# Performance work log

Measured on AMD Instinct MI355X. Metric: run time of the kernel, lower is better.

## Reference

```python
import jax, jax.numpy as jnp
import numpy as np

HEAD_DIM = 128
NEG_INF = -1e10


def setup_inputs() -> dict:
    key = jax.random.key(0)
    k1, k2, k3, k4 = jax.random.split(key, 4)
    B, T, C, D = 4, 4096, 1024, HEAD_DIM
    x = jax.random.normal(k1, (B, T, C), dtype=jnp.float32)
    # nn.Linear(C, D, bias=False) weight is [D, C]; we store transposed [C, D]
    Wq = jax.random.normal(k2, (C, D), dtype=jnp.float32) * (1.0 / np.sqrt(C))
    Wk = jax.random.normal(k3, (C, D), dtype=jnp.float32) * (1.0 / np.sqrt(C))
    Wv = jax.random.normal(k4, (C, D), dtype=jnp.float32) * (1.0 / np.sqrt(C))
    return {"x": x, "Wq": Wq, "Wk": Wk, "Wv": Wv}


def reference(x, Wq, Wk, Wv):
    B, T, C = x.shape
    D = Wq.shape[1]
    Q = jnp.einsum("btc,cd->btd", x, Wq)
    K = jnp.einsum("btc,cd->btd", x, Wk)
    V = jnp.einsum("btc,cd->btd", x, Wv)
    scores = jnp.einsum("bqd,bkd->bqk", Q, K) * (1.0 / np.sqrt(D))
    causal = jnp.tril(jnp.ones((T, T), dtype=bool))  # [T, T]
    scores = jnp.where(causal, scores, NEG_INF)
    probs = jax.nn.softmax(scores, axis=-1)
    out = jnp.einsum("bqk,bkd->bqd", probs, V)
    return out
```

## Files before the change

kernel.cpp:

```cpp
#include <hip/hip_runtime.h>
#include <hip/hip_bf16.h>
#include <stdint.h>
#include <math.h>


typedef __attribute__((ext_vector_type(4))) float f32x4;
typedef __attribute__((ext_vector_type(8))) short bf16x8;
typedef __attribute__((ext_vector_type(4))) unsigned short u16x4;

#define NBATCH 4
#define NT 4096
#define NC 1024
#define ND 128
#define BT (NBATCH * NT)
#define NSPLIT 8
#define KSPAN (NT / NSPLIT)

#define EXP2F(x) __builtin_amdgcn_exp2f(x)

__device__ __forceinline__ unsigned short f2bf(float f) {
  union { float f; uint32_t u; } v; v.f = f;
  uint32_t u = v.u;
  return (unsigned short)((u + 0x7FFFu + ((u >> 16) & 1u)) >> 16);
}

__device__ __forceinline__ float bf2f(unsigned short h) {
  union { uint32_t u; float f; } v; v.u = ((uint32_t)h) << 16;
  return v.f;
}

__device__ __forceinline__ bf16x8 cvt8(const f32x4 a0, const f32x4 a1) {
  bf16x8 r;
  r[0] = (short)f2bf(a0[0]); r[1] = (short)f2bf(a0[1]);
  r[2] = (short)f2bf(a0[2]); r[3] = (short)f2bf(a0[3]);
  r[4] = (short)f2bf(a1[0]); r[5] = (short)f2bf(a1[1]);
  r[6] = (short)f2bf(a1[2]); r[7] = (short)f2bf(a1[3]);
  return r;
}

__device__ __forceinline__ void g2lds16(const void* g, void* l) {
  __builtin_amdgcn_global_load_lds(
      (const __attribute__((address_space(1))) unsigned int*)g,
      (__attribute__((address_space(3))) unsigned int*)l, 16, 0, 0);
}

__global__ void wcvt_kernel(const float* __restrict__ Wq, const float* __restrict__ Wk,
                            const float* __restrict__ Wv, unsigned short* __restrict__ Wt) {
  const float CK = 0.12751744f;
  int idx = blockIdx.x * blockDim.x + threadIdx.x;
  int m = idx >> 17;
  int r = idx & 131071;
  int d = r >> 10;
  int c = r & 1023;
  const float* W = (m == 0) ? Wq : (m == 1) ? Wk : Wv;
  float v = W[c * ND + d];
  if (m == 1) v *= CK;
  Wt[idx] = f2bf(v);
}

__global__ __launch_bounds__(256, 3)
void proj_kernel(const float* __restrict__ x, const unsigned short* __restrict__ Wt,
                 unsigned short* __restrict__ Qb, unsigned short* __restrict__ Kb,
                 unsigned short* __restrict__ Vt) {
  __shared__ char smem[2][16384];

  int w = threadIdx.x >> 6;
  int lane = threadIdx.x & 63;
  int r16 = lane & 15;
  int h4 = lane >> 4;
  int wm = w & 1;
  int wn = w >> 1;

  int mt = blockIdx.x & 255;
  int nt = blockIdx.x >> 8;

  const char* xg = (const char*)(x + (size_t)(mt * 64) * NC);
  const char* wg = (const char*)(Wt + (size_t)(nt * 128) * NC);

  f32x4 acc[2][4];
  #pragma unroll
  for (int m = 0; m < 2; ++m)
    #pragma unroll
    for (int n = 0; n < 4; ++n) acc[m][n] = (f32x4){0.f, 0.f, 0.f, 0.f};

  int cA0 = (w * 2 + 0) * 64 + lane;
  int cA1 = (w * 2 + 1) * 64 + lane;

  #define STAGE(buf, t)                                                          \
    {                                                                            \
      int c0 = (t) * 32;                                                         \
      {                                                                          \
        int c = cA0, row = c >> 3, s = c & 7;                                    \
        g2lds16(xg + (size_t)row * 4096 + c0 * 4 + ((s ^ (row & 7)) << 4),       \
                smem[buf] + (w * 2 + 0) * 1024);                                 \
      }                                                                          \
      {                                                                          \
        int c = cA1, row = c >> 3, s = c & 7;                                    \
        g2lds16(xg + (size_t)row * 4096 + c0 * 4 + ((s ^ (row & 7)) << 4),       \
                smem[buf] + (w * 2 + 1) * 1024);                                 \
      }                                                                          \
      {                                                                          \
        int c = cA0, row = c >> 2, s = c & 3;                                    \
        g2lds16(wg + (size_t)row * 2048 + c0 * 2 + ((s ^ (row & 3)) << 4),       \
                smem[buf] + 8192 + (w * 2 + 0) * 1024);                          \
      }                                                                          \
      {                                                                          \
        int c = cA1, row = c >> 2, s = c & 3;                                    \
        g2lds16(wg + (size_t)row * 2048 + c0 * 2 + ((s ^ (row & 3)) << 4),       \
                smem[buf] + 8192 + (w * 2 + 1) * 1024);                          \
      }                                                                          \
    }

  STAGE(0, 0);
  __syncthreads();

  for (int t = 0; t < 32; ++t) {
    int cur = t & 1;
    if (t + 1 < 32) STAGE(cur ^ 1, t + 1);

    bf16x8 af[2];
    #pragma unroll
    for (int m = 0; m < 2; ++m) {
      int row = wm * 32 + m * 16 + r16;
      f32x4 a0 = *(const f32x4*)(smem[cur] + row * 128 + (((h4 * 2) ^ (row & 7)) << 4));
      f32x4 a1 = *(const f32x4*)(smem[cur] + row * 128 + (((h4 * 2 + 1) ^ (row & 7)) << 4));
      af[m] = cvt8(a0, a1);
    }
    __builtin_amdgcn_s_setprio(1);
    #pragma unroll
    for (int n = 0; n < 4; ++n) {
      int brow = wn * 64 + n * 16 + r16;
      bf16x8 bfr = *(const bf16x8*)(smem[cur] + 8192 + brow * 64 + ((h4 ^ (brow & 3)) << 4));
      acc[0][n] = __builtin_amdgcn_mfma_f32_16x16x32_bf16(af[0], bfr, acc[0][n], 0, 0, 0);
      acc[1][n] = __builtin_amdgcn_mfma_f32_16x16x32_bf16(af[1], bfr, acc[1][n], 0, 0, 0);
    }
    __builtin_amdgcn_s_setprio(0);
    __syncthreads();
  }
  #undef STAGE

  if (nt < 2) {
    unsigned short* dst = (nt == 0) ? Qb : Kb;
    #pragma unroll
    for (int m = 0; m < 2; ++m) {
      int t0 = mt * 64 + wm * 32 + m * 16 + h4 * 4;
      #pragma unroll
      for (int n = 0; n < 4; ++n) {
        int d = wn * 64 + n * 16 + r16;
        #pragma unroll
        for (int r = 0; r < 4; ++r)
          dst[(size_t)(t0 + r) * ND + d] = f2bf(acc[m][n][r]);
      }
    }
  } else {
    #pragma unroll
    for (int m = 0; m < 2; ++m) {
      int t0 = mt * 64 + wm * 32 + m * 16 + h4 * 4;
      int b = t0 >> 12;
      int tl = t0 & (NT - 1);
      #pragma unroll
      for (int n = 0; n < 4; ++n) {
        int d = wn * 64 + n * 16 + r16;
        u16x4 pk;
        #pragma unroll
        for (int r = 0; r < 4; ++r) pk[r] = f2bf(acc[m][n][r]);
        *(u16x4*)(Vt + (size_t)b * (ND * NT) + (size_t)d * NT + tl) = pk;
      }
    }
  }
}

__global__ __launch_bounds__(256, 2)
void attn_kernel(const unsigned short* __restrict__ Qb,
                 const unsigned short* __restrict__ Kb,
                 const unsigned short* __restrict__ Vt,
                 unsigned short* __restrict__ Opart, float* __restrict__ Mpart,
                 float* __restrict__ Lpart) {
  __shared__ unsigned short kbuf[64 * 128];
  __shared__ unsigned short vbuf[128 * 64];
  __shared__ unsigned short plds[4][32][72];

  int wave = threadIdx.x >> 6;
  int lane = threadIdx.x & 63;
  int r16 = lane & 15;
  int h4 = lane >> 4;
  int h8 = h4 * 8;

  int l = blockIdx.x;
  int b = l & 3;
  int u = l >> 2;
  int a = (int)((sqrtf(2.0f * (float)u + 1.0f) - 1.0f) * 0.5f);
  if (a < 0) a = 0;
  while (2 * (a + 1) * (a + 2) <= u) ++a;
  while (a > 0 && 2 * a * (a + 1) > u) --a;
  int rem = u - 2 * a * (a + 1);
  int apl = a + 1;
  int rr = rem / apl;
  int s = rem - rr * apl;
  int qbt = 4 * a + rr;

  int qb0 = qbt * 128;
  int z = s;
  int kstart = s << 9;
  int kend = min(qb0 + 128, kstart + KSPAN);

  int q0 = qb0 + wave * 32;

  const unsigned short* Qbb = Qb + (size_t)b * NT * ND;
  const unsigned short* Kbb = Kb + (size_t)b * NT * ND;
  const unsigned short* Vtb = Vt + (size_t)b * ND * NT;

  bf16x8 qf[2][4];
  #pragma unroll
  for (int f = 0; f < 2; ++f)
    #pragma unroll
    for (int dc = 0; dc < 4; ++dc)
      qf[f][dc] = *(const bf16x8*)(Qbb + (size_t)(q0 + f * 16 + r16) * ND + dc * 32 + h8);

  f32x4 accO[2][8];
  #pragma unroll
  for (int f = 0; f < 2; ++f)
    #pragma unroll
    for (int i = 0; i < 8; ++i) accO[f][i] = (f32x4){0.f, 0.f, 0.f, 0.f};
  float mr[2][4], lr[2][4];
  #pragma unroll
  for (int f = 0; f < 2; ++f)
    #pragma unroll
    for (int r = 0; r < 4; ++r) { mr[f][r] = -1e30f; lr[f][r] = 0.f; }

  for (int kv0 = kstart; kv0 < kend; kv0 += 64) {
    #pragma unroll
    for (int i = 0; i < 4; ++i) {
      int e = i * 256 + wave * 64 + lane;
      int krow = e >> 4, ks = e & 15;
      const char* gk = (const char*)(Kbb + (size_t)(kv0 + krow) * ND)
                       + ((ks * 16) ^ ((krow & 7) << 4));
      g2lds16(gk, (char*)kbuf + (size_t)(i * 256 + wave * 64) * 16);
    }
    #pragma unroll
    for (int i = 0; i < 4; ++i) {
      int e = i * 256 + wave * 64 + lane;
      int vrow = e >> 3, vs = e & 7;
      const char* gv = (const char*)(Vtb + (size_t)vrow * NT + kv0)
                       + ((vs * 16) ^ ((vrow & 7) << 4));
      g2lds16(gv, (char*)vbuf + (size_t)(i * 256 + wave * 64) * 16);
    }
    __syncthreads();

    if (kv0 < q0 + 32) {
      f32x4 s2[2][4];
      __builtin_amdgcn_s_setprio(1);
      #pragma unroll
      for (int kt = 0; kt < 4; ++kt) {
        s2[0][kt] = (f32x4){0.f, 0.f, 0.f, 0.f};
        s2[1][kt] = (f32x4){0.f, 0.f, 0.f, 0.f};
        int krow = kt * 16 + r16;
        #pragma unroll
        for (int dc = 0; dc < 4; ++dc) {
          int off = krow * 256 + ((dc * 64 + h4 * 16) ^ ((krow & 7) << 4));
          bf16x8 kf = *(const bf16x8*)((const char*)kbuf + off);
          s2[0][kt] = __builtin_amdgcn_mfma_f32_16x16x32_bf16(qf[0][dc], kf, s2[0][kt], 0, 0, 0);
          s2[1][kt] = __builtin_amdgcn_mfma_f32_16x16x32_bf16(qf[1][dc], kf, s2[1][kt], 0, 0, 0);
        }
      }
      __builtin_amdgcn_s_setprio(0);

      float pmax[2][4];
      #pragma unroll
      for (int f = 0; f < 2; ++f)
        #pragma unroll
        for (int r = 0; r < 4; ++r) pmax[f][r] = -3e38f;
      if (kv0 + 63 <= q0) {
        #pragma unroll
        for (int kt = 0; kt < 4; ++kt)
          #pragma unroll
          for (int f = 0; f < 2; ++f)
            #pragma unroll
            for (int r = 0; r < 4; ++r) pmax[f][r] = fmaxf(pmax[f][r], s2[f][kt][r]);
      } else {
        #pragma unroll
        for (int kt = 0; kt < 4; ++kt) {
          int key = kv0 + kt * 16 + r16;
          #pragma unroll
          for (int f = 0; f < 2; ++f)
            #pragma unroll
            for (int r = 0; r < 4; ++r) {
              int q = q0 + f * 16 + h4 * 4 + r;
              float v = (key <= q) ? s2[f][kt][r] : -3e38f;
              s2[f][kt][r] = v;
              pmax[f][r] = fmaxf(pmax[f][r], v);
            }
        }
      }

      bool grow = false;
      #pragma unroll
      for (int f = 0; f < 2; ++f)
        #pragma unroll
        for (int r = 0; r < 4; ++r) grow = grow || (pmax[f][r] > mr[f][r] + 11.0f);
      if (__any(grow)) {
        #pragma unroll
        for (int f = 0; f < 2; ++f) {
          float sf[4];
          #pragma unroll
          for (int r = 0; r < 4; ++r) {
            #pragma unroll
            for (int msk = 1; msk < 16; msk <<= 1)
              pmax[f][r] = fmaxf(pmax[f][r], __shfl_xor(pmax[f][r], msk, 64));
            float mn = fmaxf(mr[f][r], pmax[f][r]);
            sf[r] = EXP2F(mr[f][r] - mn);
            mr[f][r] = mn;
            lr[f][r] *= sf[r];
          }
          #pragma unroll
          for (int dt = 0; dt < 8; ++dt) {
            #pragma unroll
            for (int r = 0; r < 4; ++r) accO[f][dt][r] *= sf[r];
          }
        }
      }

      #pragma unroll
      for (int kt = 0; kt < 4; ++kt)
        #pragma unroll
        for (int f = 0; f < 2; ++f)
          #pragma unroll
          for (int r = 0; r < 4; ++r) {
            float p = EXP2F(s2[f][kt][r] - mr[f][r]);
            s2[f][kt][r] = p;
            lr[f][r] += p;
          }

      #pragma unroll
      for (int kt = 0; kt < 4; ++kt)
        #pragma unroll
        for (int f = 0; f < 2; ++f)
          #pragma unroll
          for (int r = 0; r < 4; ++r)
            plds[wave][f * 16 + h4 * 4 + r][kt * 16 + r16] = f2bf(s2[f][kt][r]);

      __builtin_amdgcn_s_setprio(1);
      #pragma unroll
      for (int kc = 0; kc < 2; ++kc) {
        bf16x8 pf0 = *(const bf16x8*)(&plds[wave][r16][kc * 32 + h8]);
        bf16x8 pf1 = *(const bf16x8*)(&plds[wave][16 + r16][kc * 32 + h8]);
        #pragma unroll
        for (int dt = 0; dt < 8; ++dt) {
          int vrow = dt * 16 + r16;
          int off = vrow * 128 + ((kc * 64 + h4 * 16) ^ ((vrow & 7) << 4));
          bf16x8 vf = *(const bf16x8*)((const char*)vbuf + off);
          accO[0][dt] = __builtin_amdgcn_mfma_f32_16x16x32_bf16(pf0, vf, accO[0][dt], 0, 0, 0);
          accO[1][dt] = __builtin_amdgcn_mfma_f32_16x16x32_bf16(pf1, vf, accO[1][dt], 0, 0, 0);
        }
      }
      __builtin_amdgcn_s_setprio(0);
    }
    __syncthreads();
  }

  #pragma unroll
  for (int f = 0; f < 2; ++f)
    #pragma unroll
    for (int r = 0; r < 4; ++r)
      #pragma unroll
      for (int msk = 1; msk < 16; msk <<= 1)
        lr[f][r] += __shfl_xor(lr[f][r], msk, 64);

  size_t pbase = ((size_t)z * NBATCH + b) * NT + q0;
  #pragma unroll
  for (int f = 0; f < 2; ++f)
    #pragma unroll
    for (int dt = 0; dt < 8; ++dt)
      #pragma unroll
      for (int r = 0; r < 4; ++r)
        Opart[(pbase + f * 16 + h4 * 4 + r) * ND + dt * 16 + r16] = f2bf(accO[f][dt][r]);
  if (r16 == 0) {
    #pragma unroll
    for (int f = 0; f < 2; ++f)
      #pragma unroll
      for (int r = 0; r < 4; ++r) {
        Mpart[pbase + f * 16 + h4 * 4 + r] = mr[f][r];
        Lpart[pbase + f * 16 + h4 * 4 + r] = lr[f][r];
      }
  }
}

__global__ void merge_kernel(const unsigned short* __restrict__ Opart,
                             const float* __restrict__ Mpart,
                             const float* __restrict__ Lpart, float* __restrict__ out) {
  int idx = blockIdx.x * blockDim.x + threadIdx.x;
  int bq = idx >> 4;
  int dg = idx & 15;
  int q = bq & (NT - 1);
  int nz = (q >> 9) + 1;

  float M = -3e38f;
  #pragma unroll
  for (int zz = 0; zz < NSPLIT; ++zz)
    if (zz < nz) M = fmaxf(M, Mpart[(size_t)zz * BT + bq]);

  float denom = 0.f;
  float o[8] = {0.f, 0.f, 0.f, 0.f, 0.f, 0.f, 0.f, 0.f};
  #pragma unroll
  for (int zz = 0; zz < NSPLIT; ++zz) {
    if (zz < nz) {
      float e = EXP2F(Mpart[(size_t)zz * BT + bq] - M);
      denom += e * Lpart[(size_t)zz * BT + bq];
      bf16x8 ov = *(const bf16x8*)(Opart + ((size_t)zz * BT + bq) * ND + dg * 8);
      #pragma unroll
      for (int j = 0; j < 8; ++j) o[j] += e * bf2f((unsigned short)ov[j]);
    }
  }
  float inv = 1.0f / denom;
  f32x4 o0, o1;
  #pragma unroll
  for (int j = 0; j < 4; ++j) { o0[j] = o[j] * inv; o1[j] = o[4 + j] * inv; }
  float* dst = out + (size_t)bq * ND + dg * 8;
  *(f32x4*)dst = o0;
  *(f32x4*)(dst + 4) = o1;
}

extern "C" void kernel_launch(void* const* d_in, const int* in_sizes, int n_in,
                              void* d_out, int out_size, void* d_ws, size_t ws_size,
                              hipStream_t stream) {
  const float* x  = (const float*)d_in[0];
  const float* Wq = (const float*)d_in[1];
  const float* Wk = (const float*)d_in[2];
  const float* Wv = (const float*)d_in[3];

  char* ws = (char*)d_ws;
  unsigned short* Qb = (unsigned short*)ws;
  unsigned short* Kb = (unsigned short*)(ws + 4194304);
  unsigned short* Vt = (unsigned short*)(ws + 8388608);
  unsigned short* Opart = (unsigned short*)(ws + 12582912);
  float* Mpart = (float*)(ws + 46137344);
  float* Lpart = (float*)(ws + 46661632);
  unsigned short* Wt = (unsigned short*)(ws + 12582912);

  hipLaunchKernelGGL(wcvt_kernel, dim3(1536), dim3(256), 0, stream, Wq, Wk, Wv, Wt);
  hipLaunchKernelGGL(proj_kernel, dim3(768), dim3(256), 0, stream, x, Wt, Qb, Kb, Vt);
  hipLaunchKernelGGL(attn_kernel, dim3(576), dim3(256), 0, stream,
                     Qb, Kb, Vt, Opart, Mpart, Lpart);
  hipLaunchKernelGGL(merge_kernel, dim3(BT * 16 / 256), dim3(256), 0, stream,
                     Opart, Mpart, Lpart, (float*)d_out);
}
```

Before: 86.38 us.

## Map waves to batches and read K/V fragments directly from global memory

```diff
diff --git a/kernel.cpp b/kernel.cpp
--- a/kernel.cpp
+++ b/kernel.cpp
@@ -176,8 +176,6 @@
                  const unsigned short* __restrict__ Vt,
                  unsigned short* __restrict__ Opart, float* __restrict__ Mpart,
                  float* __restrict__ Lpart) {
-  __shared__ unsigned short kbuf[64 * 128];
-  __shared__ unsigned short vbuf[128 * 64];
   __shared__ unsigned short plds[4][32][72];
 
   int wave = threadIdx.x >> 6;
@@ -186,25 +184,20 @@
   int h4 = lane >> 4;
   int h8 = h4 * 8;
 
-  int l = blockIdx.x;
-  int b = l & 3;
-  int u = l >> 2;
-  int a = (int)((sqrtf(2.0f * (float)u + 1.0f) - 1.0f) * 0.5f);
-  if (a < 0) a = 0;
-  while (2 * (a + 1) * (a + 2) <= u) ++a;
-  while (a > 0 && 2 * a * (a + 1) > u) --a;
-  int rem = u - 2 * a * (a + 1);
-  int apl = a + 1;
-  int rr = rem / apl;
-  int s = rem - rr * apl;
-  int qbt = 4 * a + rr;
-
-  int qb0 = qbt * 128;
+  int b = wave;
+  int u = blockIdx.x;
+  int g = (int)((sqrtf(4.0f + 2.0f * (float)u) - 2.0f) * 0.25f);
+  if (g < 0) g = 0;
+  while (8 * (g + 1) * (g + 2) <= u) ++g;
+  while (g > 0 && 8 * g * (g + 1) > u) --g;
+  int rem = u - 8 * g * (g + 1);
+  int qt = 16 * g + rem / (g + 1);
+  int s = rem % (g + 1);
+
+  int q0 = qt * 32;
   int z = s;
   int kstart = s << 9;
-  int kend = min(qb0 + 128, kstart + KSPAN);
-
-  int q0 = qb0 + wave * 32;
+  int kend = min(q0 + 32, kstart + KSPAN);
 
   const unsigned short* Qbb = Qb + (size_t)b * NT * ND;
   const unsigned short* Kbb = Kb + (size_t)b * NT * ND;
@@ -229,133 +222,109 @@
     for (int r = 0; r < 4; ++r) { mr[f][r] = -1e30f; lr[f][r] = 0.f; }
 
   for (int kv0 = kstart; kv0 < kend; kv0 += 64) {
-    #pragma unroll
-    for (int i = 0; i < 4; ++i) {
-      int e = i * 256 + wave * 64 + lane;
-      int krow = e >> 4, ks = e & 15;
-      const char* gk = (const char*)(Kbb + (size_t)(kv0 + krow) * ND)
-                       + ((ks * 16) ^ ((krow & 7) << 4));
-      g2lds16(gk, (char*)kbuf + (size_t)(i * 256 + wave * 64) * 16);
-    }
-    #pragma unroll
-    for (int i = 0; i < 4; ++i) {
-      int e = i * 256 + wave * 64 + lane;
-      int vrow = e >> 3, vs = e & 7;
-      const char* gv = (const char*)(Vtb + (size_t)vrow * NT + kv0)
-                       + ((vs * 16) ^ ((vrow & 7) << 4));
-      g2lds16(gv, (char*)vbuf + (size_t)(i * 256 + wave * 64) * 16);
-    }
-    __syncthreads();
-
-    if (kv0 < q0 + 32) {
-      f32x4 s2[2][4];
-      __builtin_amdgcn_s_setprio(1);
+    f32x4 s2[2][4];
+    __builtin_amdgcn_s_setprio(1);
+    #pragma unroll
+    for (int kt = 0; kt < 4; ++kt) {
+      s2[0][kt] = (f32x4){0.f, 0.f, 0.f, 0.f};
+      s2[1][kt] = (f32x4){0.f, 0.f, 0.f, 0.f};
+      const unsigned short* krow = Kbb + (size_t)(kv0 + kt * 16 + r16) * ND;
+      #pragma unroll
+      for (int dc = 0; dc < 4; ++dc) {
+        bf16x8 kf = *(const bf16x8*)(krow + dc * 32 + h8);
+        s2[0][kt] = __builtin_amdgcn_mfma_f32_16x16x32_bf16(qf[0][dc], kf, s2[0][kt], 0, 0, 0);
+        s2[1][kt] = __builtin_amdgcn_mfma_f32_16x16x32_bf16(qf[1][dc], kf, s2[1][kt], 0, 0, 0);
+      }
+    }
+    __builtin_amdgcn_s_setprio(0);
+
+    float pmax[2][4];
+    #pragma unroll
+    for (int f = 0; f < 2; ++f)
+      #pragma unroll
+      for (int r = 0; r < 4; ++r) pmax[f][r] = -3e38f;
+    if (kv0 + 63 <= q0) {
+      #pragma unroll
+      for (int kt = 0; kt < 4; ++kt)
+        #pragma unroll
+        for (int f = 0; f < 2; ++f)
+          #pragma unroll
+          for (int r = 0; r < 4; ++r) pmax[f][r] = fmaxf(pmax[f][r], s2[f][kt][r]);
+    } else {
       #pragma unroll
       for (int kt = 0; kt < 4; ++kt) {
-        s2[0][kt] = (f32x4){0.f, 0.f, 0.f, 0.f};
-        s2[1][kt] = (f32x4){0.f, 0.f, 0.f, 0.f};
-        int krow = kt * 16 + r16;
-        #pragma unroll
-        for (int dc = 0; dc < 4; ++dc) {
-          int off = krow * 256 + ((dc * 64 + h4 * 16) ^ ((krow & 7) << 4));
-          bf16x8 kf = *(const bf16x8*)((const char*)kbuf + off);
-          s2[0][kt] = __builtin_amdgcn_mfma_f32_16x16x32_bf16(qf[0][dc], kf, s2[0][kt], 0, 0, 0);
-          s2[1][kt] = __builtin_amdgcn_mfma_f32_16x16x32_bf16(qf[1][dc], kf, s2[1][kt], 0, 0, 0);
-        }
-      }
-      __builtin_amdgcn_s_setprio(0);
-
-      float pmax[2][4];
-      #pragma unroll
-      for (int f = 0; f < 2; ++f)
-        #pragma unroll
-        for (int r = 0; r < 4; ++r) pmax[f][r] = -3e38f;
-      if (kv0 + 63 <= q0) {
-        #pragma unroll
-        for (int kt = 0; kt < 4; ++kt)
-          #pragma unroll
-          for (int f = 0; f < 2; ++f)
-            #pragma unroll
-            for (int r = 0; r < 4; ++r) pmax[f][r] = fmaxf(pmax[f][r], s2[f][kt][r]);
-      } else {
-        #pragma unroll
-        for (int kt = 0; kt < 4; ++kt) {
-          int key = kv0 + kt * 16 + r16;
-          #pragma unroll
-          for (int f = 0; f < 2; ++f)
-            #pragma unroll
-            for (int r = 0; r < 4; ++r) {
-              int q = q0 + f * 16 + h4 * 4 + r;
-              float v = (key <= q) ? s2[f][kt][r] : -3e38f;
-              s2[f][kt][r] = v;
-              pmax[f][r] = fmaxf(pmax[f][r], v);
-            }
-        }
-      }
-
-      bool grow = false;
-      #pragma unroll
-      for (int f = 0; f < 2; ++f)
-        #pragma unroll
-        for (int r = 0; r < 4; ++r) grow = grow || (pmax[f][r] > mr[f][r] + 11.0f);
-      if (__any(grow)) {
-        #pragma unroll
-        for (int f = 0; f < 2; ++f) {
-          float sf[4];
-          #pragma unroll
-          for (int r = 0; r < 4; ++r) {
-            #pragma unroll
-            for (int msk = 1; msk < 16; msk <<= 1)
-              pmax[f][r] = fmaxf(pmax[f][r], __shfl_xor(pmax[f][r], msk, 64));
-            float mn = fmaxf(mr[f][r], pmax[f][r]);
-            sf[r] = EXP2F(mr[f][r] - mn);
-            mr[f][r] = mn;
-            lr[f][r] *= sf[r];
-          }
-          #pragma unroll
-          for (int dt = 0; dt < 8; ++dt) {
-            #pragma unroll
-            for (int r = 0; r < 4; ++r) accO[f][dt][r] *= sf[r];
-          }
-        }
-      }
-
-      #pragma unroll
-      for (int kt = 0; kt < 4; ++kt)
+        int key = kv0 + kt * 16 + r16;
         #pragma unroll
         for (int f = 0; f < 2; ++f)
           #pragma unroll
           for (int r = 0; r < 4; ++r) {
-            float p = EXP2F(s2[f][kt][r] - mr[f][r]);
-            s2[f][kt][r] = p;
-            lr[f][r] += p;
+            int q = q0 + f * 16 + h4 * 4 + r;
+            float v = (key <= q) ? s2[f][kt][r] : -3e38f;
+            s2[f][kt][r] = v;
+            pmax[f][r] = fmaxf(pmax[f][r], v);
           }
-
-      #pragma unroll
-      for (int kt = 0; kt < 4; ++kt)
-        #pragma unroll
-        for (int f = 0; f < 2; ++f)
+      }
+    }
+
+    bool grow = false;
+    #pragma unroll
+    for (int f = 0; f < 2; ++f)
+      #pragma unroll
+      for (int r = 0; r < 4; ++r) grow = grow || (pmax[f][r] > mr[f][r] + 11.0f);
+    if (__any(grow)) {
+      #pragma unroll
+      for (int f = 0; f < 2; ++f) {
+        float sf[4];
+        #pragma unroll
+        for (int r = 0; r < 4; ++r) {
           #pragma unroll
-          for (int r = 0; r < 4; ++r)
-            plds[wave][f * 16 + h4 * 4 + r][kt * 16 + r16] = f2bf(s2[f][kt][r]);
-
-      __builtin_amdgcn_s_setprio(1);
-      #pragma unroll
-      for (int kc = 0; kc < 2; ++kc) {
-        bf16x8 pf0 = *(const bf16x8*)(&plds[wave][r16][kc * 32 + h8]);
-        bf16x8 pf1 = *(const bf16x8*)(&plds[wave][16 + r16][kc * 32 + h8]);
+          for (int msk = 1; msk < 16; msk <<= 1)
+            pmax[f][r] = fmaxf(pmax[f][r], __shfl_xor(pmax[f][r], msk, 64));
+          float mn = fmaxf(mr[f][r], pmax[f][r]);
+          sf[r] = EXP2F(mr[f][r] - mn);
+          mr[f][r] = mn;
+          lr[f][r] *= sf[r];
+        }
         #pragma unroll
         for (int dt = 0; dt < 8; ++dt) {
-          int vrow = dt * 16 + r16;
-          int off = vrow * 128 + ((kc * 64 + h4 * 16) ^ ((vrow & 7) << 4));
-          bf16x8 vf = *(const bf16x8*)((const char*)vbuf + off);
-          accO[0][dt] = __builtin_amdgcn_mfma_f32_16x16x32_bf16(pf0, vf, accO[0][dt], 0, 0, 0);
-          accO[1][dt] = __builtin_amdgcn_mfma_f32_16x16x32_bf16(pf1, vf, accO[1][dt], 0, 0, 0);
+          #pragma unroll
+          for (int r = 0; r < 4; ++r) accO[f][dt][r] *= sf[r];
         }
       }
-      __builtin_amdgcn_s_setprio(0);
-    }
-    __syncthreads();
+    }
+
+    #pragma unroll
+    for (int kt = 0; kt < 4; ++kt)
+      #pragma unroll
+      for (int f = 0; f < 2; ++f)
+        #pragma unroll
+        for (int r = 0; r < 4; ++r) {
+          float p = EXP2F(s2[f][kt][r] - mr[f][r]);
+          s2[f][kt][r] = p;
+          lr[f][r] += p;
+        }
+
+    #pragma unroll
+    for (int kt = 0; kt < 4; ++kt)
+      #pragma unroll
+      for (int f = 0; f < 2; ++f)
+        #pragma unroll
+        for (int r = 0; r < 4; ++r)
+          plds[wave][f * 16 + h4 * 4 + r][kt * 16 + r16] = f2bf(s2[f][kt][r]);
+
+    __builtin_amdgcn_s_setprio(1);
+    #pragma unroll
+    for (int kc = 0; kc < 2; ++kc) {
+      bf16x8 pf0 = *(const bf16x8*)(&plds[wave][r16][kc * 32 + h8]);
+      bf16x8 pf1 = *(const bf16x8*)(&plds[wave][16 + r16][kc * 32 + h8]);
+      #pragma unroll
+      for (int dt = 0; dt < 8; ++dt) {
+        bf16x8 vf = *(const bf16x8*)(Vtb + (size_t)(dt * 16 + r16) * NT + kv0 + kc * 32 + h8);
+        accO[0][dt] = __builtin_amdgcn_mfma_f32_16x16x32_bf16(pf0, vf, accO[0][dt], 0, 0, 0);
+        accO[1][dt] = __builtin_amdgcn_mfma_f32_16x16x32_bf16(pf1, vf, accO[1][dt], 0, 0, 0);
+      }
+    }
+    __builtin_amdgcn_s_setprio(0);
   }
 
   #pragma unroll
```

Measured after the change: 154.1 us. +78.4%, slower.

## Compute transposed score tiles so softmax row stats live per lane

Applied to the files above, without the earlier changes.

```diff
diff --git a/kernel.cpp b/kernel.cpp
--- a/kernel.cpp
+++ b/kernel.cpp
@@ -7,6 +7,7 @@
 typedef __attribute__((ext_vector_type(4))) float f32x4;
 typedef __attribute__((ext_vector_type(8))) short bf16x8;
 typedef __attribute__((ext_vector_type(4))) unsigned short u16x4;
+typedef __attribute__((ext_vector_type(2))) unsigned int u32x2;
 
 #define NBATCH 4
 #define NT 4096
@@ -35,6 +36,12 @@
   r[2] = (short)f2bf(a0[2]); r[3] = (short)f2bf(a0[3]);
   r[4] = (short)f2bf(a1[0]); r[5] = (short)f2bf(a1[1]);
   r[6] = (short)f2bf(a1[2]); r[7] = (short)f2bf(a1[3]);
+  return r;
+}
+
+__device__ __forceinline__ unsigned int cvtpk(float a, float b) {
+  unsigned int r;
+  asm("v_cvt_pk_bf16_f32 %0, %1, %2" : "=v"(r) : "v"(a), "v"(b));
   return r;
 }
 
@@ -222,11 +229,8 @@
   for (int f = 0; f < 2; ++f)
     #pragma unroll
     for (int i = 0; i < 8; ++i) accO[f][i] = (f32x4){0.f, 0.f, 0.f, 0.f};
-  float mr[2][4], lr[2][4];
-  #pragma unroll
-  for (int f = 0; f < 2; ++f)
-    #pragma unroll
-    for (int r = 0; r < 4; ++r) { mr[f][r] = -1e30f; lr[f][r] = 0.f; }
+  float mr[2] = {-1e30f, -1e30f};
+  float lr[2] = {0.f, 0.f};
 
   for (int kv0 = kstart; kv0 < kend; kv0 += 64) {
     #pragma unroll
@@ -248,96 +252,88 @@
     __syncthreads();
 
     if (kv0 < q0 + 32) {
-      f32x4 s2[2][4];
+      f32x4 sT[2][4];
       __builtin_amdgcn_s_setprio(1);
       #pragma unroll
       for (int kt = 0; kt < 4; ++kt) {
-        s2[0][kt] = (f32x4){0.f, 0.f, 0.f, 0.f};
-        s2[1][kt] = (f32x4){0.f, 0.f, 0.f, 0.f};
+        sT[0][kt] = (f32x4){0.f, 0.f, 0.f, 0.f};
+        sT[1][kt] = (f32x4){0.f, 0.f, 0.f, 0.f};
         int krow = kt * 16 + r16;
         #pragma unroll
         for (int dc = 0; dc < 4; ++dc) {
           int off = krow * 256 + ((dc * 64 + h4 * 16) ^ ((krow & 7) << 4));
           bf16x8 kf = *(const bf16x8*)((const char*)kbuf + off);
-          s2[0][kt] = __builtin_amdgcn_mfma_f32_16x16x32_bf16(qf[0][dc], kf, s2[0][kt], 0, 0, 0);
-          s2[1][kt] = __builtin_amdgcn_mfma_f32_16x16x32_bf16(qf[1][dc], kf, s2[1][kt], 0, 0, 0);
+          sT[0][kt] = __builtin_amdgcn_mfma_f32_16x16x32_bf16(kf, qf[0][dc], sT[0][kt], 0, 0, 0);
+          sT[1][kt] = __builtin_amdgcn_mfma_f32_16x16x32_bf16(kf, qf[1][dc], sT[1][kt], 0, 0, 0);
         }
       }
       __builtin_amdgcn_s_setprio(0);
 
-      float pmax[2][4];
-      #pragma unroll
-      for (int f = 0; f < 2; ++f)
-        #pragma unroll
-        for (int r = 0; r < 4; ++r) pmax[f][r] = -3e38f;
+      float pmax[2] = {-3e38f, -3e38f};
       if (kv0 + 63 <= q0) {
         #pragma unroll
         for (int kt = 0; kt < 4; ++kt)
           #pragma unroll
           for (int f = 0; f < 2; ++f)
             #pragma unroll
-            for (int r = 0; r < 4; ++r) pmax[f][r] = fmaxf(pmax[f][r], s2[f][kt][r]);
+            for (int r = 0; r < 4; ++r) pmax[f] = fmaxf(pmax[f], sT[f][kt][r]);
       } else {
         #pragma unroll
         for (int kt = 0; kt < 4; ++kt) {
-          int key = kv0 + kt * 16 + r16;
+          int kb = kv0 + kt * 16 + h4 * 4;
           #pragma unroll
-          for (int f = 0; f < 2; ++f)
+          for (int f = 0; f < 2; ++f) {
+            int q = q0 + f * 16 + r16;
             #pragma unroll
             for (int r = 0; r < 4; ++r) {
-              int q = q0 + f * 16 + h4 * 4 + r;
-              float v = (key <= q) ? s2[f][kt][r] : -3e38f;
-              s2[f][kt][r] = v;
-              pmax[f][r] = fmaxf(pmax[f][r], v);
+              float v = (kb + r <= q) ? sT[f][kt][r] : -3e38f;
+              sT[f][kt][r] = v;
+              pmax[f] = fmaxf(pmax[f], v);
             }
+          }
         }
       }
 
-      bool grow = false;
-      #pragma unroll
-      for (int f = 0; f < 2; ++f)
-        #pragma unroll
-        for (int r = 0; r < 4; ++r) grow = grow || (pmax[f][r] > mr[f][r] + 11.0f);
+      bool grow = (pmax[0] > mr[0] + 11.0f) || (pmax[1] > mr[1] + 11.0f);
       if (__any(grow)) {
+        float sf[2], sfa[2][4];
         #pragma unroll
         for (int f = 0; f < 2; ++f) {
-          float sf[4];
+          pmax[f] = fmaxf(pmax[f], __shfl_xor(pmax[f], 16, 64));
+          pmax[f] = fmaxf(pmax[f], __shfl_xor(pmax[f], 32, 64));
+          float mn = fmaxf(mr[f], pmax[f]);
+          sf[f] = EXP2F(mr[f] - mn);
+          mr[f] = mn;
+          lr[f] *= sf[f];
+        }
+        #pragma unroll
+        for (int f = 0; f < 2; ++f)
           #pragma unroll
-          for (int r = 0; r < 4; ++r) {
-            #pragma unroll
-            for (int msk = 1; msk < 16; msk <<= 1)
-              pmax[f][r] = fmaxf(pmax[f][r], __shfl_xor(pmax[f][r], msk, 64));
-            float mn = fmaxf(mr[f][r], pmax[f][r]);
-            sf[r] = EXP2F(mr[f][r] - mn);
-            mr[f][r] = mn;
-            lr[f][r] *= sf[r];
-          }
+          for (int r = 0; r < 4; ++r) sfa[f][r] = __shfl(sf[f], h4 * 4 + r, 64);
+        #pragma unroll
+        for (int f = 0; f < 2; ++f)
           #pragma unroll
           for (int dt = 0; dt < 8; ++dt) {
             #pragma unroll
-            for (int r = 0; r < 4; ++r) accO[f][dt][r] *= sf[r];
+            for (int r = 0; r < 4; ++r) accO[f][dt][r] *= sfa[f][r];
           }
+      }
+
+      #pragma unroll
+      for (int f = 0; f < 2; ++f) {
+        #pragma unroll
+        for (int kt = 0; kt < 4; ++kt) {
+          float p0 = EXP2F(sT[f][kt][0] - mr[f]);
+          float p1 = EXP2F(sT[f][kt][1] - mr[f]);
+          float p2 = EXP2F(sT[f][kt][2] - mr[f]);
+          float p3 = EXP2F(sT[f][kt][3] - mr[f]);
+          lr[f] += (p0 + p1) + (p2 + p3);
+          u32x2 pk;
+          pk[0] = cvtpk(p0, p1);
+          pk[1] = cvtpk(p2, p3);
+          *(u32x2*)&plds[wave][f * 16 + r16][kt * 16 + h4 * 4] = pk;
         }
       }
-
-      #pragma unroll
-      for (int kt = 0; kt < 4; ++kt)
-        #pragma unroll
-        for (int f = 0; f < 2; ++f)
-          #pragma unroll
-          for (int r = 0; r < 4; ++r) {
-            float p = EXP2F(s2[f][kt][r] - mr[f][r]);
-            s2[f][kt][r] = p;
-            lr[f][r] += p;
-          }
-
-      #pragma unroll
-      for (int kt = 0; kt < 4; ++kt)
-        #pragma unroll
-        for (int f = 0; f < 2; ++f)
-          #pragma unroll
-          for (int r = 0; r < 4; ++r)
-            plds[wave][f * 16 + h4 * 4 + r][kt * 16 + r16] = f2bf(s2[f][kt][r]);
 
       __builtin_amdgcn_s_setprio(1);
       #pragma unroll
@@ -359,12 +355,10 @@
   }
 
   #pragma unroll
-  for (int f = 0; f < 2; ++f)
-    #pragma unroll
-    for (int r = 0; r < 4; ++r)
-      #pragma unroll
-      for (int msk = 1; msk < 16; msk <<= 1)
-        lr[f][r] += __shfl_xor(lr[f][r], msk, 64);
+  for (int f = 0; f < 2; ++f) {
+    lr[f] += __shfl_xor(lr[f], 16, 64);
+    lr[f] += __shfl_xor(lr[f], 32, 64);
+  }
 
   size_t pbase = ((size_t)z * NBATCH + b) * NT + q0;
   #pragma unroll
@@ -374,14 +368,12 @@
       #pragma unroll
       for (int r = 0; r < 4; ++r)
         Opart[(pbase + f * 16 + h4 * 4 + r) * ND + dt * 16 + r16] = f2bf(accO[f][dt][r]);
-  if (r16 == 0) {
-    #pragma unroll
-    for (int f = 0; f < 2; ++f)
-      #pragma unroll
-      for (int r = 0; r < 4; ++r) {
-        Mpart[pbase + f * 16 + h4 * 4 + r] = mr[f][r];
-        Lpart[pbase + f * 16 + h4 * 4 + r] = lr[f][r];
-      }
+  if (h4 == 0) {
+    #pragma unroll
+    for (int f = 0; f < 2; ++f) {
+      Mpart[pbase + f * 16 + r16] = mr[f];
+      Lpart[pbase + f * 16 + r16] = lr[f];
+    }
   }
 }
 
```

Result: faster. 79.74 us (-7.7%).
